# Kernel optimization log

Hardware: AMD Instinct MI355X
Metric: run time of the kernel (lower is better)

## Reference

```python
import jax, jax.numpy as jnp
import numpy as np
from jax import lax

B, L, H = 2, 1024, 2048
E, N, TR, K = 4096, 16, 128, 4


def setup_inputs() -> dict:
    key = jax.random.key(0)
    ks = jax.random.split(key, 10)
    s = lambda d: 1.0 / np.sqrt(d)
    return {
        "input_states": jax.random.normal(ks[0], (B, L, H), jnp.float32),
        "W_in": jax.random.normal(ks[1], (H, 2 * E), jnp.float32) * s(H),
        "conv_kernel": jax.random.normal(ks[2], (E, 1, K), jnp.float32) * s(K),
        "conv_bias": jax.random.normal(ks[3], (E,), jnp.float32) * 0.01,
        "W_x": jax.random.normal(ks[4], (E, TR + 2 * N), jnp.float32) * s(E),
        "W_dt": jax.random.normal(ks[5], (TR, E), jnp.float32) * s(TR),
        "b_dt": jax.random.normal(ks[6], (E,), jnp.float32) * 0.01,
        "W_out": jax.random.normal(ks[7], (E, H), jnp.float32) * s(E),
        "A_log": jax.random.uniform(ks[8], (E, N), jnp.float32, 0.0, 2.0),
        "D": jax.random.normal(ks[9], (E,), jnp.float32),
    }


def reference(input_states, W_in, conv_kernel, conv_bias, W_x, W_dt, b_dt,
              W_out, A_log, D):
    b, l, _ = input_states.shape
    dtype = input_states.dtype
    # in projection -> (b, 2E, l), split into hidden and gate streams
    proj = jnp.einsum("blh,he->bel", input_states, W_in)
    hidden, gate = jnp.split(proj, 2, axis=1)  # each (b, E, l)
    # depthwise causal conv1d (pad K-1, trim to l) + SiLU
    x = lax.conv_general_dilated(hidden, conv_kernel, window_strides=(1,),
                                 padding=((K - 1, K - 1),),
                                 feature_group_count=E)[..., :l]
    hidden = jax.nn.silu(x + conv_bias[None, :, None])  # (b, E, l)
    hs_ble = hidden.transpose(0, 2, 1)  # (b, l, E)
    # SSM parameters: dt (b,l,TR), Bm (b,l,N), Cm (b,l,N)
    ssm_p = jnp.einsum("ble,ed->bld", hs_ble, W_x)
    dt, Bm, Cm = jnp.split(ssm_p, [TR, TR + N], axis=-1)
    dts = jax.nn.softplus(jnp.einsum("blr,re->ble", dt, W_dt) + b_dt)  # (b,l,E)
    A = -jnp.exp(A_log.astype(jnp.float32))  # (E, N)
    # discretization
    dA = jnp.exp(dts[..., None] * A[None, None])            # (b, l, E, N)
    dBu = dts[..., None] * Bm[:, :, None, :] * hs_ble[..., None]  # (b, l, E, N)
    # selective scan over time (time-major for lax.scan)
    def step(state, inp):
        a, bu, c = inp  # (b,E,N), (b,E,N), (b,N)
        state = a * state + bu
        y = jnp.einsum("ben,bn->be", state.astype(dtype), c)
        return state, y
    init = jnp.zeros((b, E, N), dtype=dtype)
    _, ys = lax.scan(step, init, (dA.transpose(1, 0, 2, 3),
                                  dBu.transpose(1, 0, 2, 3),
                                  Cm.transpose(1, 0, 2)))  # ys: (l, b, E)
    scan_out = ys.transpose(1, 2, 0)  # (b, E, l)
    y = (scan_out + hidden * D[None, :, None]) * jax.nn.silu(gate)
    return jnp.einsum("bel,eh->blh", y, W_out)
```

## Files before the change

### kernel.cpp

```cpp
#include <hip/hip_runtime.h>
#include <cstddef>
#include <cstdint>

constexpr int B_  = 2;
constexpr int L_  = 1024;
constexpr int H_  = 2048;
constexpr int E_  = 4096;
constexpr int N_  = 16;
constexpr int TR_ = 128;
constexpr int M_  = B_ * L_;
constexpr int P2E = 2 * E_;
constexpr int SLD = TR_ + 2 * N_;
constexpr int CH_ = 32;
constexpr int CL_ = L_ / CH_;

typedef unsigned short u16;
using short8 = __attribute__((ext_vector_type(8))) short;
using f32x4  = __attribute__((ext_vector_type(4))) float;

__device__ __forceinline__ float siluf(float x) { return x / (1.f + expf(-x)); }
__device__ __forceinline__ float silu_fast(float x) { return x / (1.f + __expf(-x)); }
__device__ __forceinline__ float softplusf(float x) {
  return fmaxf(x, 0.f) + log1pf(expf(-fabsf(x)));
}
__device__ __forceinline__ u16 f2bf(float x) {
  union { float f; uint32_t u; } v; v.f = x;
  uint32_t r = v.u + 0x7FFFu + ((v.u >> 16) & 1u);
  return (u16)(r >> 16);
}
__device__ __forceinline__ float bf2f(u16 h) {
  union { uint32_t u; float f; } v; v.u = ((uint32_t)h) << 16; return v.f;
}

template<int BM, int BN, int BK, int TM, int TN, int EPI>
__global__ __launch_bounds__(256) void sgemm_k(
    const float* __restrict__ A, const float* __restrict__ B,
    float* __restrict__ C, int lda, int ldb, int ldc,
    const float* __restrict__ bias, int kchunk)
{
  __shared__ float As[BK][BM + 4];
  __shared__ float Bs[BK][BN];
  const int tid = threadIdx.x;
  const int tx  = tid & 15;
  const int ty  = tid >> 4;
  const int m0  = blockIdx.y * BM;
  const int n0  = blockIdx.x * BN;
  const int k00 = blockIdx.z * kchunk;

  float acc[TM][TN];
#pragma unroll
  for (int i = 0; i < TM; ++i)
#pragma unroll
    for (int j = 0; j < TN; ++j) acc[i][j] = 0.f;

  for (int k0 = k00; k0 < k00 + kchunk; k0 += BK) {
    constexpr int A4 = BM * BK / 4;
#pragma unroll
    for (int it = 0; it < (A4 + 255) / 256; ++it) {
      int i = it * 256 + tid;
      if ((A4 % 256 == 0) || (i < A4)) {
        int row = i / (BK / 4);
        int kc  = (i % (BK / 4)) * 4;
        float4 v = *reinterpret_cast<const float4*>(
            A + (size_t)(m0 + row) * lda + k0 + kc);
        As[kc + 0][row] = v.x; As[kc + 1][row] = v.y;
        As[kc + 2][row] = v.z; As[kc + 3][row] = v.w;
      }
    }
    constexpr int B4 = BK * BN / 4;
#pragma unroll
    for (int it = 0; it < (B4 + 255) / 256; ++it) {
      int i = it * 256 + tid;
      if ((B4 % 256 == 0) || (i < B4)) {
        int kr = i / (BN / 4);
        int nc = (i % (BN / 4)) * 4;
        *reinterpret_cast<float4*>(&Bs[kr][nc]) =
            *reinterpret_cast<const float4*>(
                B + (size_t)(k0 + kr) * ldb + n0 + nc);
      }
    }
    __syncthreads();
#pragma unroll
    for (int k = 0; k < BK; ++k) {
      float a[TM], bb[TN];
      const float* ap = &As[k][ty * TM];
      if constexpr (TM == 8) {
        float4 a0 = *reinterpret_cast<const float4*>(ap);
        float4 a1 = *reinterpret_cast<const float4*>(ap + 4);
        a[0]=a0.x; a[1]=a0.y; a[2]=a0.z; a[3]=a0.w;
        a[4]=a1.x; a[5]=a1.y; a[6]=a1.z; a[7]=a1.w;
      } else {
        float4 a0 = *reinterpret_cast<const float4*>(ap);
        a[0]=a0.x; a[1]=a0.y; a[2]=a0.z; a[3]=a0.w;
      }
      const float* bp = &Bs[k][tx * TN];
      if constexpr (TN == 4) {
        float4 b0 = *reinterpret_cast<const float4*>(bp);
        bb[0]=b0.x; bb[1]=b0.y; bb[2]=b0.z; bb[3]=b0.w;
      } else {
        float2 b0 = *reinterpret_cast<const float2*>(bp);
        bb[0]=b0.x; bb[1]=b0.y;
      }
#pragma unroll
      for (int i = 0; i < TM; ++i)
#pragma unroll
        for (int j = 0; j < TN; ++j) acc[i][j] = fmaf(a[i], bb[j], acc[i][j]);
    }
    __syncthreads();
  }

#pragma unroll
  for (int i = 0; i < TM; ++i) {
    int row = m0 + ty * TM + i;
    float* crow = C + (size_t)row * ldc + n0 + tx * TN;
    if constexpr (EPI == 2) {
#pragma unroll
      for (int j = 0; j < TN; ++j) atomicAdd(&crow[j], acc[i][j]);
    } else if constexpr (EPI == 1) {
      const float* brow = bias + n0 + tx * TN;
      float4 v;
      v.x = softplusf(acc[i][0] + brow[0]);
      v.y = softplusf(acc[i][1] + brow[1]);
      v.z = softplusf(acc[i][2] + brow[2]);
      v.w = softplusf(acc[i][3] + brow[3]);
      *reinterpret_cast<float4*>(crow) = v;
    } else {
      if constexpr (TN == 4) {
        float4 v; v.x=acc[i][0]; v.y=acc[i][1]; v.z=acc[i][2]; v.w=acc[i][3];
        *reinterpret_cast<float4*>(crow) = v;
      } else {
#pragma unroll
        for (int j = 0; j < TN; ++j) crow[j] = acc[i][j];
      }
    }
  }
}

__global__ __launch_bounds__(256) void decomp_k(
    const float* __restrict__ in, u16* __restrict__ hi, u16* __restrict__ lo,
    int n4)
{
  int i = blockIdx.x * 256 + threadIdx.x;
  if (i >= n4) return;
  float4 v = *reinterpret_cast<const float4*>(in + (size_t)i * 4);
  u16 h[4], l[4];
  float x[4] = {v.x, v.y, v.z, v.w};
#pragma unroll
  for (int j = 0; j < 4; ++j) {
    h[j] = f2bf(x[j]);
    l[j] = f2bf(x[j] - bf2f(h[j]));
  }
  uint32_t h0 = h[0] | ((uint32_t)h[1] << 16), h1 = h[2] | ((uint32_t)h[3] << 16);
  uint32_t l0 = l[0] | ((uint32_t)l[1] << 16), l1 = l[2] | ((uint32_t)l[3] << 16);
  *reinterpret_cast<uint2*>(hi + (size_t)i * 4) = make_uint2(h0, h1);
  *reinterpret_cast<uint2*>(lo + (size_t)i * 4) = make_uint2(l0, l1);
}

__global__ __launch_bounds__(256) void wdecomp_t_k(
    const float* __restrict__ W, u16* __restrict__ Whi, u16* __restrict__ Wlo,
    int KD, int ND)
{
  __shared__ float T[64][69];
  const int t  = threadIdx.x;
  const int n0 = blockIdx.x * 64;
  const int k0 = blockIdx.y * 64;
#pragma unroll
  for (int it = 0; it < 4; ++it) {
    int f  = it * 256 + t;
    int kk = f >> 4;
    int c  = (f & 15) * 4;
    float4 v = *reinterpret_cast<const float4*>(
        W + (size_t)(k0 + kk) * ND + n0 + c);
    T[kk][c] = v.x; T[kk][c+1] = v.y; T[kk][c+2] = v.z; T[kk][c+3] = v.w;
  }
  __syncthreads();
  const int nn   = t >> 2;
  const int kseg = (t & 3) * 16;
  const size_t off = (size_t)(n0 + nn) * KD + k0 + kseg;
#pragma unroll
  for (int half = 0; half < 2; ++half) {
    uint32_t hp[4], lp[4];
#pragma unroll
    for (int jj = 0; jj < 4; ++jj) {
      float x0 = T[kseg + half * 8 + jj * 2 + 0][nn];
      float x1 = T[kseg + half * 8 + jj * 2 + 1][nn];
      u16 h0 = f2bf(x0), h1 = f2bf(x1);
      u16 l0 = f2bf(x0 - bf2f(h0)), l1 = f2bf(x1 - bf2f(h1));
      hp[jj] = h0 | ((uint32_t)h1 << 16);
      lp[jj] = l0 | ((uint32_t)l1 << 16);
    }
    *reinterpret_cast<uint4*>(Whi + off + half * 8) =
        make_uint4(hp[0], hp[1], hp[2], hp[3]);
    *reinterpret_cast<uint4*>(Wlo + off + half * 8) =
        make_uint4(lp[0], lp[1], lp[2], lp[3]);
  }
}

__global__ __launch_bounds__(256) void gemm3bf_k(
    const u16* __restrict__ Ah, const u16* __restrict__ Al,
    const u16* __restrict__ Bh, const u16* __restrict__ Bl,
    float* __restrict__ C, int K, int ldc)
{
  constexpr int BK  = 32;
  constexpr int LDK = BK + 8;
  __shared__ __align__(16) u16 sAh[128 * LDK];
  __shared__ __align__(16) u16 sAl[128 * LDK];
  __shared__ __align__(16) u16 sBh[128 * LDK];
  __shared__ __align__(16) u16 sBl[128 * LDK];

  const int tid  = threadIdx.x;
  const int lane = tid & 63;
  const int wid  = tid >> 6;
  const int wr   = wid >> 1, wc = wid & 1;
  const int m0   = blockIdx.y * 128;
  const int n0   = blockIdx.x * 128;

  const int r0 = tid >> 2;
  const int c0 = (tid & 3) * 8;

  const u16* gAh0 = Ah + (size_t)(m0 + r0) * K + c0;
  const u16* gAh1 = Ah + (size_t)(m0 + r0 + 64) * K + c0;
  const u16* gAl0 = Al + (size_t)(m0 + r0) * K + c0;
  const u16* gAl1 = Al + (size_t)(m0 + r0 + 64) * K + c0;
  const u16* gBh0 = Bh + (size_t)(n0 + r0) * K + c0;
  const u16* gBh1 = Bh + (size_t)(n0 + r0 + 64) * K + c0;
  const u16* gBl0 = Bl + (size_t)(n0 + r0) * K + c0;
  const u16* gBl1 = Bl + (size_t)(n0 + r0 + 64) * K + c0;

  const int s0 = r0 * LDK + c0;
  const int s1 = (r0 + 64) * LDK + c0;

  f32x4 acc[4][4] = {};

  const int fr = lane & 15;
  const int fk = (lane >> 4) * 8;

  for (int k0 = 0; k0 < K; k0 += BK) {
    uint4 vah0 = *reinterpret_cast<const uint4*>(gAh0 + k0);
    uint4 vah1 = *reinterpret_cast<const uint4*>(gAh1 + k0);
    uint4 val0 = *reinterpret_cast<const uint4*>(gAl0 + k0);
    uint4 val1 = *reinterpret_cast<const uint4*>(gAl1 + k0);
    uint4 vbh0 = *reinterpret_cast<const uint4*>(gBh0 + k0);
    uint4 vbh1 = *reinterpret_cast<const uint4*>(gBh1 + k0);
    uint4 vbl0 = *reinterpret_cast<const uint4*>(gBl0 + k0);
    uint4 vbl1 = *reinterpret_cast<const uint4*>(gBl1 + k0);
    __syncthreads();
    *reinterpret_cast<uint4*>(&sAh[s0]) = vah0;
    *reinterpret_cast<uint4*>(&sAh[s1]) = vah1;
    *reinterpret_cast<uint4*>(&sAl[s0]) = val0;
    *reinterpret_cast<uint4*>(&sAl[s1]) = val1;
    *reinterpret_cast<uint4*>(&sBh[s0]) = vbh0;
    *reinterpret_cast<uint4*>(&sBh[s1]) = vbh1;
    *reinterpret_cast<uint4*>(&sBl[s0]) = vbl0;
    *reinterpret_cast<uint4*>(&sBl[s1]) = vbl1;
    __syncthreads();

    short8 bhf[4], blf[4];
#pragma unroll
    for (int nc = 0; nc < 4; ++nc) {
      int row = wc * 64 + nc * 16 + fr;
      bhf[nc] = *reinterpret_cast<const short8*>(&sBh[row * LDK + fk]);
      blf[nc] = *reinterpret_cast<const short8*>(&sBl[row * LDK + fk]);
    }
#pragma unroll
    for (int mr = 0; mr < 4; ++mr) {
      int row = wr * 64 + mr * 16 + fr;
      short8 ahf = *reinterpret_cast<const short8*>(&sAh[row * LDK + fk]);
      short8 alf = *reinterpret_cast<const short8*>(&sAl[row * LDK + fk]);
#pragma unroll
      for (int nc = 0; nc < 4; ++nc) {
        acc[mr][nc] = __builtin_amdgcn_mfma_f32_16x16x32_bf16(ahf, bhf[nc], acc[mr][nc], 0, 0, 0);
        acc[mr][nc] = __builtin_amdgcn_mfma_f32_16x16x32_bf16(ahf, blf[nc], acc[mr][nc], 0, 0, 0);
        acc[mr][nc] = __builtin_amdgcn_mfma_f32_16x16x32_bf16(alf, bhf[nc], acc[mr][nc], 0, 0, 0);
      }
    }
  }

#pragma unroll
  for (int mr = 0; mr < 4; ++mr) {
    const int rowb = m0 + wr * 64 + mr * 16 + ((lane >> 4) << 2);
#pragma unroll
    for (int nc = 0; nc < 4; ++nc) {
      const int col = n0 + wc * 64 + nc * 16 + fr;
      float* cp = C + (size_t)rowb * ldc + col;
#pragma unroll
      for (int i = 0; i < 4; ++i) cp[(size_t)i * ldc] = acc[mr][nc][i];
    }
  }
}

__global__ __launch_bounds__(256) void conv_silu_k(
    const float* __restrict__ proj, const float* __restrict__ ck,
    const float* __restrict__ cb, float* __restrict__ hc)
{
  const int idx = blockIdx.x * 256 + threadIdx.x;
  const int e = idx & (E_ - 1);
  const int m = idx >> 12;
  const int l = m & (L_ - 1);
  const float c0 = ck[e * 4 + 0], c1 = ck[e * 4 + 1];
  const float c2 = ck[e * 4 + 2], c3 = ck[e * 4 + 3];
  const float* pcol = proj + (size_t)m * P2E + e;
  float acc = cb[e];
  if (l >= 3) acc = fmaf(pcol[-3 * P2E], c0, acc);
  if (l >= 2) acc = fmaf(pcol[-2 * P2E], c1, acc);
  if (l >= 1) acc = fmaf(pcol[-1 * P2E], c2, acc);
  acc = fmaf(pcol[0], c3, acc);
  hc[(size_t)m * E_ + e] = siluf(acc);
}

__global__ __launch_bounds__(256) void scan_p1_k(
    const float* __restrict__ hc, const float* __restrict__ ssm,
    const float* __restrict__ A_log, const float* __restrict__ dts,
    float* __restrict__ Pbuf, float* __restrict__ Qbuf)
{
  __shared__ float sB[CL_][16];
  const int tid = threadIdx.x;
  const int bid = blockIdx.x;
  const int e   = ((bid & 15) << 8) + tid;
  const int c   = (bid >> 4) & (CH_ - 1);
  const int b   = bid >> 9;
  const int m0  = b * L_ + c * CL_;

  if (tid < CL_ * 4) {
    int s = tid >> 2, q = tid & 3;
    *reinterpret_cast<float4*>(&sB[s][q * 4]) =
        *reinterpret_cast<const float4*>(
            &ssm[(size_t)(m0 + s) * SLD + TR_ + q * 4]);
  }
  __syncthreads();

  float Aen[N_];
#pragma unroll
  for (int q = 0; q < 4; ++q) {
    float4 av = *reinterpret_cast<const float4*>(&A_log[e * N_ + q * 4]);
    Aen[q*4+0] = -expf(av.x); Aen[q*4+1] = -expf(av.y);
    Aen[q*4+2] = -expf(av.z); Aen[q*4+3] = -expf(av.w);
  }

  float P[N_], Q[N_];
#pragma unroll
  for (int n = 0; n < N_; ++n) { P[n] = 1.f; Q[n] = 0.f; }

  float dt_c = dts[(size_t)m0 * E_ + e];
  float h_c  = hc [(size_t)m0 * E_ + e];
  for (int s = 0; s < CL_; ++s) {
    const int sn = (s + 1 < CL_) ? s + 1 : s;
    const float dt_n = dts[(size_t)(m0 + sn) * E_ + e];
    const float h_n  = hc [(size_t)(m0 + sn) * E_ + e];
    const float dth = dt_c * h_c;
#pragma unroll
    for (int q = 0; q < 4; ++q) {
      const float4 bv = *reinterpret_cast<const float4*>(&sB[s][q * 4]);
      const float bx[4] = {bv.x, bv.y, bv.z, bv.w};
#pragma unroll
      for (int j = 0; j < 4; ++j) {
        const int n = q * 4 + j;
        const float a = __expf(dt_c * Aen[n]);
        Q[n] = fmaf(a, Q[n], dth * bx[j]);
        P[n] *= a;
      }
    }
    dt_c = dt_n; h_c = h_n;
  }

  const size_t ob = (((size_t)b * CH_ + c) * N_) * E_ + e;
#pragma unroll
  for (int n = 0; n < N_; ++n) {
    Pbuf[ob + (size_t)n * E_] = P[n];
    Qbuf[ob + (size_t)n * E_] = Q[n];
  }
}

__global__ __launch_bounds__(256) void scan_p3_k(
    const float* __restrict__ hc, const float* __restrict__ ssm,
    const float* __restrict__ proj, const float* __restrict__ A_log,
    const float* __restrict__ Dvec, const float* __restrict__ dts,
    const float* __restrict__ Pbuf, const float* __restrict__ Qbuf,
    u16* __restrict__ yhi, u16* __restrict__ ylo)
{
  __shared__ float sBC[CL_][32];
  const int tid = threadIdx.x;
  const int bid = blockIdx.x;
  const int e   = ((bid & 15) << 8) + tid;
  const int c   = (bid >> 4) & (CH_ - 1);
  const int b   = bid >> 9;
  const int m0  = b * L_ + c * CL_;

  {
    int s = tid >> 3, q = tid & 7;
    *reinterpret_cast<float4*>(&sBC[s][q * 4]) =
        *reinterpret_cast<const float4*>(
            &ssm[(size_t)(m0 + s) * SLD + TR_ + q * 4]);
  }
  __syncthreads();

  float Aen[N_];
#pragma unroll
  for (int q = 0; q < 4; ++q) {
    float4 av = *reinterpret_cast<const float4*>(&A_log[e * N_ + q * 4]);
    Aen[q*4+0] = -expf(av.x); Aen[q*4+1] = -expf(av.y);
    Aen[q*4+2] = -expf(av.z); Aen[q*4+3] = -expf(av.w);
  }
  const float De = Dvec[e];

  float st[N_];
#pragma unroll
  for (int n = 0; n < N_; ++n) st[n] = 0.f;
  for (int cc = 0; cc < c; ++cc) {
    const size_t ob = (((size_t)b * CH_ + cc) * N_) * E_ + e;
#pragma unroll
    for (int n = 0; n < N_; ++n)
      st[n] = fmaf(Pbuf[ob + (size_t)n * E_], st[n], Qbuf[ob + (size_t)n * E_]);
  }

  float dt_c = dts[(size_t)m0 * E_ + e];
  float h_c  = hc [(size_t)m0 * E_ + e];
  float g_c  = proj[(size_t)m0 * P2E + E_ + e];
  for (int s = 0; s < CL_; ++s) {
    const int sn = (s + 1 < CL_) ? s + 1 : s;
    const float dt_n = dts[(size_t)(m0 + sn) * E_ + e];
    const float h_n  = hc [(size_t)(m0 + sn) * E_ + e];
    const float g_n  = proj[(size_t)(m0 + sn) * P2E + E_ + e];
    const float dth = dt_c * h_c;
    float y = h_c * De;
#pragma unroll
    for (int q = 0; q < 4; ++q) {
      const float4 bv = *reinterpret_cast<const float4*>(&sBC[s][q * 4]);
      const float4 cv = *reinterpret_cast<const float4*>(&sBC[s][16 + q * 4]);
      const float bx[4] = {bv.x, bv.y, bv.z, bv.w};
      const float cx[4] = {cv.x, cv.y, cv.z, cv.w};
#pragma unroll
      for (int j = 0; j < 4; ++j) {
        const int n = q * 4 + j;
        const float a = __expf(dt_c * Aen[n]);
        st[n] = fmaf(a, st[n], dth * bx[j]);
        y = fmaf(st[n], cx[j], y);
      }
    }
    const float res = y * silu_fast(g_c);
    const u16 hv = f2bf(res);
    const size_t yo = (size_t)(m0 + s) * E_ + e;
    yhi[yo] = hv;
    ylo[yo] = f2bf(res - bf2f(hv));
    dt_c = dt_n; h_c = h_n; g_c = g_n;
  }
}

__global__ __launch_bounds__(256) void scan_serial_k(
    const float* __restrict__ hc, const float* __restrict__ ssm,
    const float* __restrict__ proj, const float* __restrict__ A_log,
    const float* __restrict__ Dvec, const float* __restrict__ dts,
    float* __restrict__ yf)
{
  const int tid = threadIdx.x;
  const int n  = tid & 15;
  const int ge = blockIdx.x * 16 + (tid >> 4);
  const int b  = ge >> 12;
  const int e  = ge & (E_ - 1);
  const float Aen = -expf(A_log[e * N_ + n]);
  const float De  = Dvec[e];
  float state = 0.f;
  const int mbase = b * L_;
  for (int l = 0; l < L_; ++l) {
    const int m = mbase + l;
    const float dt = dts[(size_t)m * E_ + e];
    const float h  = hc[(size_t)m * E_ + e];
    const float Bm = ssm[(size_t)m * SLD + TR_ + n];
    const float Cm = ssm[(size_t)m * SLD + TR_ + N_ + n];
    state = fmaf(expf(dt * Aen), state, dt * Bm * h);
    float yp = state * Cm;
    yp += __shfl_xor(yp, 1);
    yp += __shfl_xor(yp, 2);
    yp += __shfl_xor(yp, 4);
    yp += __shfl_xor(yp, 8);
    const float g   = proj[(size_t)m * P2E + E_ + e];
    const float res = (yp + h * De) * siluf(g);
    if (n == 0) yf[(size_t)m * E_ + e] = res;
  }
}

extern "C" void kernel_launch(void* const* d_in, const int* in_sizes, int n_in,
                              void* d_out, int out_size, void* d_ws, size_t ws_size,
                              hipStream_t stream)
{
  const float* x_in  = (const float*)d_in[0];
  const float* W_in  = (const float*)d_in[1];
  const float* ck    = (const float*)d_in[2];
  const float* cb    = (const float*)d_in[3];
  const float* W_x   = (const float*)d_in[4];
  const float* W_dt  = (const float*)d_in[5];
  const float* b_dt  = (const float*)d_in[6];
  const float* W_out = (const float*)d_in[7];
  const float* A_log = (const float*)d_in[8];
  const float* Dvec  = (const float*)d_in[9];
  float* out = (float*)d_out;
  float* ws  = (float*)d_ws;

  float* proj = ws;
  float* hc   = proj + (size_t)M_ * P2E;
  float* dts  = hc   + (size_t)M_ * E_;
  float* ssm  = dts  + (size_t)M_ * E_;

  u16* regA  = (u16*)(ssm + (size_t)M_ * SLD);
  u16* x_hi  = regA;
  u16* x_lo  = regA + (size_t)M_ * H_;
  u16* Wo_hi = regA;
  u16* Wo_lo = regA + (size_t)H_ * E_;
  u16* regB  = regA + 16777216;
  u16* Wi_hi = regB;
  u16* Wi_lo = regB + (size_t)P2E * H_;
  u16* y_hi  = regB;
  u16* y_lo  = regB + (size_t)M_ * E_;
  float* Pbuf = (float*)(regB + 16777216);
  float* Qbuf = Pbuf + (size_t)B_ * CH_ * E_ * N_;

  const size_t need_bf =
      ((size_t)M_ * P2E + 2 * (size_t)M_ * E_ + (size_t)M_ * SLD) * 4 +
      (16777216ULL + 33554432ULL) * 2;

  hipMemsetAsync(ssm, 0, (size_t)M_ * SLD * sizeof(float), stream);

  if (ws_size >= need_bf) {
    decomp_k<<<(M_ * H_ / 4 + 255) / 256, 256, 0, stream>>>(
        x_in, x_hi, x_lo, M_ * H_ / 4);
    wdecomp_t_k<<<dim3(P2E / 64, H_ / 64), 256, 0, stream>>>(
        W_in, Wi_hi, Wi_lo, H_, P2E);
    gemm3bf_k<<<dim3(P2E / 128, M_ / 128), 256, 0, stream>>>(
        x_hi, x_lo, Wi_hi, Wi_lo, proj, H_, P2E);
    conv_silu_k<<<(M_ * E_) / 256, 256, 0, stream>>>(proj, ck, cb, hc);
    sgemm_k<64,32,16,4,2,2><<<dim3(SLD/32, M_/64, 8), 256, 0, stream>>>(
        hc, W_x, ssm, E_, SLD, SLD, nullptr, E_/8);
    sgemm_k<128,64,16,8,4,1><<<dim3(E_/64, M_/128, 1), 256, 0, stream>>>(
        ssm, W_dt, dts, SLD, E_, E_, b_dt, TR_);
    wdecomp_t_k<<<dim3(H_ / 64, E_ / 64), 256, 0, stream>>>(
        W_out, Wo_hi, Wo_lo, E_, H_);
    scan_p1_k<<<B_ * CH_ * (E_ / 256), 256, 0, stream>>>(
        hc, ssm, A_log, dts, Pbuf, Qbuf);
    scan_p3_k<<<B_ * CH_ * (E_ / 256), 256, 0, stream>>>(
        hc, ssm, proj, A_log, Dvec, dts, Pbuf, Qbuf, y_hi, y_lo);
    gemm3bf_k<<<dim3(H_ / 128, M_ / 128), 256, 0, stream>>>(
        y_hi, y_lo, Wo_hi, Wo_lo, out, E_, H_);
  } else {
    size_t base_f = (size_t)M_ * P2E + 2 * (size_t)M_ * E_ + (size_t)M_ * SLD;
    size_t need   = (base_f + (size_t)M_ * E_) * sizeof(float);
    float* yb = (ws_size >= need) ? (ssm + (size_t)M_ * SLD) : dts;
    sgemm_k<128,64,16,8,4,0><<<dim3(P2E/64, M_/128, 1), 256, 0, stream>>>(
        x_in, W_in, proj, H_, P2E, P2E, nullptr, H_);
    conv_silu_k<<<(M_ * E_) / 256, 256, 0, stream>>>(proj, ck, cb, hc);
    sgemm_k<64,32,16,4,2,2><<<dim3(SLD/32, M_/64, 8), 256, 0, stream>>>(
        hc, W_x, ssm, E_, SLD, SLD, nullptr, E_/8);
    sgemm_k<128,64,16,8,4,1><<<dim3(E_/64, M_/128, 1), 256, 0, stream>>>(
        ssm, W_dt, dts, SLD, E_, E_, b_dt, TR_);
    scan_serial_k<<<(B_ * E_) / 16, 256, 0, stream>>>(
        hc, ssm, proj, A_log, Dvec, dts, yb);
    sgemm_k<128,64,16,8,4,0><<<dim3(H_/64, M_/128, 1), 256, 0, stream>>>(
        yb, W_out, out, E_, H_, H_, nullptr, E_);
  }
}
```

Baseline: 797.5 us.

## Use direct global-to-LDS loads with XOR swizzle and XCD-aware tile remap in bf16x3 GEMM

The split-bf16 GEMM now loads tiles with global_load_lds straight into shared memory instead of staging through registers. The shared layout drops the padding and uses an XOR swizzle to avoid bank conflicts. A 1D grid is remapped so consecutive blocks spread across the 8 XCDs, with M tiles varying fastest. This is meant to cut register pressure and LDS store instructions and to improve L2 locality. The tile mapping hardcodes 16 M-tiles and a grid divisible by 8, and the loop still synchronizes without double buffering.

```diff
diff --git a/kernel.cpp b/kernel.cpp
--- a/kernel.cpp
+++ b/kernel.cpp
@@ -30,6 +30,11 @@
 }
 __device__ __forceinline__ float bf2f(u16 h) {
   union { uint32_t u; float f; } v; v.u = ((uint32_t)h) << 16; return v.f;
+}
+__device__ __forceinline__ void gll16(const u16* g, u16* l) {
+  __builtin_amdgcn_global_load_lds(
+      (const __attribute__((address_space(1))) void*)(const void*)g,
+      (__attribute__((address_space(3))) void*)(void*)l, 16, 0, 0);
 }
 
 template<int BM, int BN, int BK, int TM, int TN, int EPI>
@@ -201,72 +206,72 @@
     const u16* __restrict__ Bh, const u16* __restrict__ Bl,
     float* __restrict__ C, int K, int ldc)
 {
-  constexpr int BK  = 32;
-  constexpr int LDK = BK + 8;
-  __shared__ __align__(16) u16 sAh[128 * LDK];
-  __shared__ __align__(16) u16 sAl[128 * LDK];
-  __shared__ __align__(16) u16 sBh[128 * LDK];
-  __shared__ __align__(16) u16 sBl[128 * LDK];
+  __shared__ __align__(16) u16 sAh[128 * 32];
+  __shared__ __align__(16) u16 sAl[128 * 32];
+  __shared__ __align__(16) u16 sBh[128 * 32];
+  __shared__ __align__(16) u16 sBl[128 * 32];
 
   const int tid  = threadIdx.x;
   const int lane = tid & 63;
   const int wid  = tid >> 6;
   const int wr   = wid >> 1, wc = wid & 1;
-  const int m0   = blockIdx.y * 128;
-  const int n0   = blockIdx.x * 128;
-
-  const int r0 = tid >> 2;
-  const int c0 = (tid & 3) * 8;
-
-  const u16* gAh0 = Ah + (size_t)(m0 + r0) * K + c0;
-  const u16* gAh1 = Ah + (size_t)(m0 + r0 + 64) * K + c0;
-  const u16* gAl0 = Al + (size_t)(m0 + r0) * K + c0;
-  const u16* gAl1 = Al + (size_t)(m0 + r0 + 64) * K + c0;
-  const u16* gBh0 = Bh + (size_t)(n0 + r0) * K + c0;
-  const u16* gBh1 = Bh + (size_t)(n0 + r0 + 64) * K + c0;
-  const u16* gBl0 = Bl + (size_t)(n0 + r0) * K + c0;
-  const u16* gBl1 = Bl + (size_t)(n0 + r0 + 64) * K + c0;
-
-  const int s0 = r0 * LDK + c0;
-  const int s1 = (r0 + 64) * LDK + c0;
+
+  const int nwg = gridDim.x;
+  const int q8  = nwg >> 3;
+  const int wg  = (blockIdx.x & 7) * q8 + (blockIdx.x >> 3);
+  const int tm  = wg & 15;
+  const int tn  = wg >> 4;
+  const int m0  = tm * 128;
+  const int n0  = tn * 128;
+
+  const int dr = lane >> 2;
+  const int sw = (lane & 3) ^ ((lane >> 3) & 3);
+  const int r1 = wid * 16 + dr;
+  const int r2 = r1 + 64;
+
+  const u16* ga1 = Ah + (size_t)(m0 + r1) * K + sw * 8;
+  const u16* ga2 = Ah + (size_t)(m0 + r2) * K + sw * 8;
+  const u16* gl1 = Al + (size_t)(m0 + r1) * K + sw * 8;
+  const u16* gl2 = Al + (size_t)(m0 + r2) * K + sw * 8;
+  const u16* gb1 = Bh + (size_t)(n0 + r1) * K + sw * 8;
+  const u16* gb2 = Bh + (size_t)(n0 + r2) * K + sw * 8;
+  const u16* gc1 = Bl + (size_t)(n0 + r1) * K + sw * 8;
+  const u16* gc2 = Bl + (size_t)(n0 + r2) * K + sw * 8;
+
+  u16* dA1 = sAh + (wid * 16) * 32;
+  u16* dA2 = sAh + (64 + wid * 16) * 32;
+  u16* dL1 = sAl + (wid * 16) * 32;
+  u16* dL2 = sAl + (64 + wid * 16) * 32;
+  u16* dB1 = sBh + (wid * 16) * 32;
+  u16* dB2 = sBh + (64 + wid * 16) * 32;
+  u16* dC1 = sBl + (wid * 16) * 32;
+  u16* dC2 = sBl + (64 + wid * 16) * 32;
+
+  const int fr = lane & 15;
+  const int ph = (lane >> 4) ^ ((fr >> 1) & 3);
+  const int offA = (wr * 64 + fr) * 32 + ph * 8;
+  const int offB = (wc * 64 + fr) * 32 + ph * 8;
 
   f32x4 acc[4][4] = {};
 
-  const int fr = lane & 15;
-  const int fk = (lane >> 4) * 8;
-
-  for (int k0 = 0; k0 < K; k0 += BK) {
-    uint4 vah0 = *reinterpret_cast<const uint4*>(gAh0 + k0);
-    uint4 vah1 = *reinterpret_cast<const uint4*>(gAh1 + k0);
-    uint4 val0 = *reinterpret_cast<const uint4*>(gAl0 + k0);
-    uint4 val1 = *reinterpret_cast<const uint4*>(gAl1 + k0);
-    uint4 vbh0 = *reinterpret_cast<const uint4*>(gBh0 + k0);
-    uint4 vbh1 = *reinterpret_cast<const uint4*>(gBh1 + k0);
-    uint4 vbl0 = *reinterpret_cast<const uint4*>(gBl0 + k0);
-    uint4 vbl1 = *reinterpret_cast<const uint4*>(gBl1 + k0);
+  for (int k0 = 0; k0 < K; k0 += 32) {
     __syncthreads();
-    *reinterpret_cast<uint4*>(&sAh[s0]) = vah0;
-    *reinterpret_cast<uint4*>(&sAh[s1]) = vah1;
-    *reinterpret_cast<uint4*>(&sAl[s0]) = val0;
-    *reinterpret_cast<uint4*>(&sAl[s1]) = val1;
-    *reinterpret_cast<uint4*>(&sBh[s0]) = vbh0;
-    *reinterpret_cast<uint4*>(&sBh[s1]) = vbh1;
-    *reinterpret_cast<uint4*>(&sBl[s0]) = vbl0;
-    *reinterpret_cast<uint4*>(&sBl[s1]) = vbl1;
+    gll16(ga1 + k0, dA1);  gll16(ga2 + k0, dA2);
+    gll16(gl1 + k0, dL1);  gll16(gl2 + k0, dL2);
+    gll16(gb1 + k0, dB1);  gll16(gb2 + k0, dB2);
+    gll16(gc1 + k0, dC1);  gll16(gc2 + k0, dC2);
     __syncthreads();
 
     short8 bhf[4], blf[4];
 #pragma unroll
     for (int nc = 0; nc < 4; ++nc) {
-      int row = wc * 64 + nc * 16 + fr;
-      bhf[nc] = *reinterpret_cast<const short8*>(&sBh[row * LDK + fk]);
-      blf[nc] = *reinterpret_cast<const short8*>(&sBl[row * LDK + fk]);
+      bhf[nc] = *reinterpret_cast<const short8*>(&sBh[offB + nc * 512]);
+      blf[nc] = *reinterpret_cast<const short8*>(&sBl[offB + nc * 512]);
     }
 #pragma unroll
     for (int mr = 0; mr < 4; ++mr) {
-      int row = wr * 64 + mr * 16 + fr;
-      short8 ahf = *reinterpret_cast<const short8*>(&sAh[row * LDK + fk]);
-      short8 alf = *reinterpret_cast<const short8*>(&sAl[row * LDK + fk]);
+      short8 ahf = *reinterpret_cast<const short8*>(&sAh[offA + mr * 512]);
+      short8 alf = *reinterpret_cast<const short8*>(&sAl[offA + mr * 512]);
 #pragma unroll
       for (int nc = 0; nc < 4; ++nc) {
         acc[mr][nc] = __builtin_amdgcn_mfma_f32_16x16x32_bf16(ahf, bhf[nc], acc[mr][nc], 0, 0, 0);
@@ -525,7 +530,7 @@
         x_in, x_hi, x_lo, M_ * H_ / 4);
     wdecomp_t_k<<<dim3(P2E / 64, H_ / 64), 256, 0, stream>>>(
         W_in, Wi_hi, Wi_lo, H_, P2E);
-    gemm3bf_k<<<dim3(P2E / 128, M_ / 128), 256, 0, stream>>>(
+    gemm3bf_k<<<(M_ / 128) * (P2E / 128), 256, 0, stream>>>(
         x_hi, x_lo, Wi_hi, Wi_lo, proj, H_, P2E);
     conv_silu_k<<<(M_ * E_) / 256, 256, 0, stream>>>(proj, ck, cb, hc);
     sgemm_k<64,32,16,4,2,2><<<dim3(SLD/32, M_/64, 8), 256, 0, stream>>>(
@@ -538,7 +543,7 @@
         hc, ssm, A_log, dts, Pbuf, Qbuf);
     scan_p3_k<<<B_ * CH_ * (E_ / 256), 256, 0, stream>>>(
         hc, ssm, proj, A_log, Dvec, dts, Pbuf, Qbuf, y_hi, y_lo);
-    gemm3bf_k<<<dim3(H_ / 128, M_ / 128), 256, 0, stream>>>(
+    gemm3bf_k<<<(M_ / 128) * (H_ / 128), 256, 0, stream>>>(
         y_hi, y_lo, Wo_hi, Wo_lo, out, E_, H_);
   } else {
     size_t base_f = (size_t)M_ * P2E + 2 * (size_t)M_ * E_ + (size_t)M_ * SLD;
```

After: 832.7 us. +4.4%, slower.
